# Performance work log

Hardware: AMD Instinct MI355X
Metric: run time of the kernel (lower is better)

The kernel has to match this reference:

```python
import jax, jax.numpy as jnp
import numpy as np

B, H, W, C = 4, 48, 48, 256
NUM_HEADS = 8
DEPTH = C // NUM_HEADS  # 32


def setup_inputs() -> dict:
    key = jax.random.key(0)
    ks = jax.random.split(key, 8)
    scale = 1.0 / np.sqrt(C)
    return {
        "inputs": jax.random.normal(ks[0], (B, H, W, C), dtype=jnp.float32),
        "wq": jax.random.normal(ks[1], (C, C), dtype=jnp.float32) * scale,
        "bq": jax.random.normal(ks[2], (C,), dtype=jnp.float32) * 0.01,
        "wk": jax.random.normal(ks[3], (C, C), dtype=jnp.float32) * scale,
        "bk": jax.random.normal(ks[4], (C,), dtype=jnp.float32) * 0.01,
        "wv": jax.random.normal(ks[5], (C, C), dtype=jnp.float32) * scale,
        "bv": jax.random.normal(ks[6], (C,), dtype=jnp.float32) * 0.01,
        "gamma": jax.random.normal(ks[7], (), dtype=jnp.float32) * 0.1,
    }


def reference(inputs, wq, bq, wk, bk, wv, bv, gamma):
    b, h, w, c = inputs.shape
    n = h * w  # number of tokens

    def proj_split(wm, bm):
        # 1x1 conv == per-pixel dense: [b,h,w,c] @ [c,c] + bias
        y = jnp.einsum('bhwc,cd->bhwd', inputs, wm) + bm
        # split heads -> [b, num_heads, n, depth]
        return y.reshape(b, n, NUM_HEADS, DEPTH).transpose(0, 2, 1, 3)

    q = proj_split(wq, bq) / jnp.sqrt(jnp.asarray(DEPTH, inputs.dtype))
    k = proj_split(wk, bk)
    v = proj_split(wv, bv)

    s = jnp.einsum('bnqd,bnkd->bnqk', q, k)        # [b, heads, n, n]
    a = jax.nn.softmax(s, axis=-1)
    o = jnp.einsum('bnqk,bnkd->bnqd', a, v)        # [b, heads, n, depth]
    o = o.transpose(0, 2, 1, 3).reshape(b, h, w, c)
    return gamma * o + inputs
```

## Files before the change

### kernel.cpp

```cpp
#include <hip/hip_runtime.h>
#include <hip/hip_bf16.h>
#include <cstdint>

#define B_    4
#define NH    8
#define N_TOK 2304
#define D_    32
#define C_    256
#define M_ROWS (B_ * N_TOK)
#define KVB   64
#define NT2   (N_TOK / KVB)
#define M_FIX 10.0f

typedef float  f32x4  __attribute__((ext_vector_type(4)));
typedef short  bf16x8 __attribute__((ext_vector_type(8)));

#define GLOADLDS(g, l) __builtin_amdgcn_global_load_lds( \
    (const __attribute__((address_space(1))) unsigned*)(g), \
    (__attribute__((address_space(3))) unsigned*)(l), 16, 0, 0)

static __device__ __forceinline__ unsigned short f2bf(float f) {
    union { float f; unsigned u; } v; v.f = f;
    unsigned u = v.u;
    u += 0x7FFF + ((u >> 16) & 1);
    return (unsigned short)(u >> 16);
}

static __device__ __forceinline__ unsigned cvt_pk_bf16(float a, float b) {
    unsigned r;
    asm("v_cvt_pk_bf16_f32 %0, %1, %2" : "=v"(r) : "v"(a), "v"(b));
    return r;
}

__global__ void k_prep(const float* __restrict__ x,
                       const float* __restrict__ w0, const float* __restrict__ w1,
                       const float* __restrict__ w2,
                       unsigned short* __restrict__ xb, unsigned short* __restrict__ wt) {
    __shared__ float tile[64][65];
    int bid = blockIdx.x;
    if (bid < 2304) {
        int i = bid * 256 + threadIdx.x;
        float4 v = reinterpret_cast<const float4*>(x)[i];
        ushort4 o;
        o.x = f2bf(v.x); o.y = f2bf(v.y); o.z = f2bf(v.z); o.w = f2bf(v.w);
        reinterpret_cast<ushort4*>(xb)[i] = o;
        return;
    }
    int t   = bid - 2304;
    int mat = t >> 4;  t &= 15;
    const float* w = (mat == 0) ? w0 : (mat == 1) ? w1 : w2;
    int tc  = (t & 3) * 64;
    int td  = (t >> 2) * 64;
    int tid = threadIdx.x;
    int r0  = tid >> 6;
    int x0  = tid & 63;
#pragma unroll
    for (int it = 0; it < 16; ++it) {
        int c = it * 4 + r0;
        tile[c][x0] = w[(tc + c) * C_ + td + x0];
    }
    __syncthreads();
    unsigned short* wto = wt + mat * (C_ * C_);
#pragma unroll
    for (int it = 0; it < 16; ++it) {
        int d = it * 4 + r0;
        wto[(td + d) * C_ + tc + x0] = f2bf(tile[x0][d]);
    }
}

__global__ __launch_bounds__(256) void k_proj(
    const unsigned short* __restrict__ xb,
    const unsigned short* __restrict__ wtb,
    const float* __restrict__ bq, const float* __restrict__ bk, const float* __restrict__ bv,
    unsigned short* __restrict__ qo, unsigned short* __restrict__ kfo, unsigned short* __restrict__ vfo)
{
    __shared__ __align__(16) unsigned short A_lds[3][64][32];
    __shared__ __align__(16) unsigned short B_lds[3][128][32];

    int rows0 = blockIdx.x * 64;
    int cols0 = blockIdx.y * 128;
    int mat   = cols0 >> 8;
    const float* bias = (mat == 0) ? bq : (mat == 1) ? bk : bv;
    float scale = (mat == 0) ? (0.17677669529663687f * 1.4426950408889634f) : 1.0f;

    int tid = threadIdx.x, wave = tid >> 6, lane = tid & 63;
    int lr = lane & 15, lg = lane >> 4;
    int wr = wave >> 1, wc = wave & 1;

    int srow = lane >> 2, sslot = lane & 3;
    int ra   = wave * 16 + srow;
    int keyA = ((ra >> 1) & 1) | (((ra >> 3) & 1) << 1);
    const unsigned short* asrc = xb + (rows0 + ra) * C_ + ((sslot ^ keyA) * 8);
    int rb   = wave * 32 + srow;
    int keyB0 = ((rb >> 1) & 1) | (((rb >> 3) & 1) << 1);
    int keyB1 = (((rb + 16) >> 1) & 1) | ((((rb + 16) >> 3) & 1) << 1);
    const unsigned short* bsrc0 = wtb + (cols0 + rb) * C_ + ((sslot ^ keyB0) * 8);
    const unsigned short* bsrc1 = wtb + (cols0 + rb + 16) * C_ + ((sslot ^ keyB1) * 8);

    char* aldsb = (char*)&A_lds[0][0][0];
    char* bldsb = (char*)&B_lds[0][0][0];
    int adst = wave * 1024;
    int bdst0 = wave * 2048, bdst1 = bdst0 + 1024;

    int xorb = (((lr >> 1) & 1) << 4) | (((lr >> 3) & 1) << 5);
    int fcol = (lg * 16) ^ xorb;
    int arow0 = wr * 32 + lr;
    int brow0 = wc * 64 + lr;

#define PSTAGE(ks, bidx) do {                               \
        int ko_ = (ks) * 32;                                \
        char* ad = aldsb + (bidx) * 4096;                   \
        char* bd = bldsb + (bidx) * 8192;                   \
        GLOADLDS(asrc + ko_, ad + adst);                    \
        GLOADLDS(bsrc0 + ko_, bd + bdst0);                  \
        GLOADLDS(bsrc1 + ko_, bd + bdst1);                  \
    } while (0)

    PSTAGE(0, 0);
    PSTAGE(1, 1);
    asm volatile("s_waitcnt vmcnt(3)" ::: "memory");
    __builtin_amdgcn_s_barrier();

    f32x4 acc[2][4];
#pragma unroll
    for (int i = 0; i < 2; ++i)
#pragma unroll
        for (int j = 0; j < 4; ++j) acc[i][j] = (f32x4){0.f, 0.f, 0.f, 0.f};

    int b0 = 0;
    for (int ks = 0; ks < 8; ++ks) {
        if (ks + 2 < 8) {
            int b2 = b0 + 2; if (b2 >= 3) b2 -= 3;
            PSTAGE(ks + 2, b2);
        }
        const char* ac = aldsb + b0 * 4096;
        const char* bc = bldsb + b0 * 8192;

        bf16x8 a[2], b[4];
#pragma unroll
        for (int fr = 0; fr < 2; ++fr)
            a[fr] = *reinterpret_cast<const bf16x8*>(ac + (arow0 + fr * 16) * 64 + fcol);
#pragma unroll
        for (int fn = 0; fn < 4; ++fn)
            b[fn] = *reinterpret_cast<const bf16x8*>(bc + (brow0 + fn * 16) * 64 + fcol);

        __builtin_amdgcn_s_setprio(1);
#pragma unroll
        for (int fr = 0; fr < 2; ++fr)
#pragma unroll
            for (int fn = 0; fn < 4; ++fn)
                acc[fr][fn] = __builtin_amdgcn_mfma_f32_16x16x32_bf16(a[fr], b[fn], acc[fr][fn], 0, 0, 0);
        __builtin_amdgcn_s_setprio(0);

        if (ks < 7) {
            if (ks + 2 < 8) asm volatile("s_waitcnt vmcnt(3)" ::: "memory");
            else            asm volatile("s_waitcnt vmcnt(0)" ::: "memory");
            __builtin_amdgcn_s_barrier();
        }
        b0 = (b0 + 1 == 3) ? 0 : b0 + 1;
    }
#undef PSTAGE

    int bidx = rows0 / N_TOK;
    int nb   = rows0 - bidx * N_TOK + wr * 32 + lg * 4;

    if (mat == 2) {
#pragma unroll
        for (int fr = 0; fr < 2; ++fr)
#pragma unroll
            for (int fn = 0; fn < 4; ++fn) {
                int cm = (cols0 & 255) + wc * 64 + fn * 16 + lr;
                float bsv = bias[cm];
                int hh = cm >> 5, d = cm & 31;
                int bh = bidx * NH + hh;
                uint2 pr;
                pr.x = cvt_pk_bf16(acc[fr][fn][0] + bsv, acc[fr][fn][1] + bsv);
                pr.y = cvt_pk_bf16(acc[fr][fn][2] + bsv, acc[fr][fn][3] + bsv);
                int n0 = nb + fr * 16;
                int t = n0 >> 6, r = n0 & 63;
                int kseg = r >> 5, lgp = (r >> 3) & 3, i0 = r & 7;
                int c = kseg * 2 + (d >> 4);
                int lV = lgp * 16 + (d & 15);
                *reinterpret_cast<uint2*>(vfo + ((bh * NT2 + t) * 4 + c) * 512 + lV * 8 + i0) = pr;
            }
    } else if (mat == 1) {
#pragma unroll
        for (int fr = 0; fr < 2; ++fr)
#pragma unroll
            for (int fn = 0; fn < 4; ++fn) {
                int cm = (cols0 & 255) + wc * 64 + fn * 16 + lr;
                float bsv = bias[cm];
                int hh = cm >> 5, d = cm & 31;
                int bh = bidx * NH + hh;
#pragma unroll
                for (int j = 0; j < 4; ++j) {
                    int n = nb + fr * 16 + j;
                    int t = n >> 6, r = n & 63;
                    int kt  = ((r >> 5) << 1) | ((r >> 2) & 1);
                    int lr2 = ((r >> 3) & 3) * 4 + (r & 3);
                    int l   = (d >> 3) * 16 + lr2;
                    kfo[((bh * NT2 + t) * 4 + kt) * 512 + l * 8 + (d & 7)] =
                        f2bf(acc[fr][fn][j] + bsv);
                }
            }
    } else {
        unsigned short* dst = qo;
#pragma unroll
        for (int fr = 0; fr < 2; ++fr)
#pragma unroll
            for (int fn = 0; fn < 4; ++fn) {
                int cm = (cols0 & 255) + wc * 64 + fn * 16 + lr;
                float bsv = bias[cm];
                int hh = cm >> 5, d = cm & 31;
#pragma unroll
                for (int j = 0; j < 4; ++j) {
                    float val = (acc[fr][fn][j] + bsv) * scale;
                    dst[((bidx * NH + hh) * N_TOK + nb + fr * 16 + j) * D_ + d] = f2bf(val);
                }
            }
    }
}

__global__ __launch_bounds__(256, 3) void k_attn(
    const unsigned short* __restrict__ qb,
    const unsigned short* __restrict__ kf,
    const unsigned short* __restrict__ vf,
    const float* __restrict__ x,
    const float* __restrict__ gamma_p,
    float* __restrict__ out)
{
    int wid = (blockIdx.x & 7) * 72 + (blockIdx.x >> 3);
    int bh  = wid / 18;
    int qb0 = (wid % 18) * 128;

    int tid = threadIdx.x, wave = tid >> 6, lane = tid & 63;
    int lr = lane & 15, lg = lane >> 4;

    const unsigned short* Q  = qb + bh * N_TOK * D_;
    const unsigned short* Kb = kf + (size_t)bh * (NT2 * 4 * 512) + lane * 8;
    const unsigned short* Vb = vf + (size_t)bh * (NT2 * 4 * 512) + lane * 8;

    int qrowA = qb0 + wave * 32 + lr;
    bf16x8 qA = *reinterpret_cast<const bf16x8*>(Q + qrowA * D_ + lg * 8);
    bf16x8 qB = *reinterpret_cast<const bf16x8*>(Q + (qrowA + 16) * D_ + lg * 8);

#define LDK(dst, t, kt) dst = *reinterpret_cast<const bf16x8*>(Kb + ((t) * 4 + (kt)) * 512)
#define LDV(dst, t, c)  dst = *reinterpret_cast<const bf16x8*>(Vb + ((t) * 4 + (c)) * 512)

    bf16x8 kc0, kc1, kc2, kc3, vc0, vc1, vc2, vc3;
    LDK(kc0, 0, 0); LDK(kc1, 0, 1); LDK(kc2, 0, 2); LDK(kc3, 0, 3);
    LDV(vc0, 0, 0); LDV(vc1, 0, 1); LDV(vc2, 0, 2); LDV(vc3, 0, 3);

    f32x4 accA0 = (f32x4){0.f, 0.f, 0.f, 0.f};
    f32x4 accA1 = (f32x4){0.f, 0.f, 0.f, 0.f};
    f32x4 accB0 = (f32x4){0.f, 0.f, 0.f, 0.f};
    f32x4 accB1 = (f32x4){0.f, 0.f, 0.f, 0.f};
    f32x4 acclA = (f32x4){0.f, 0.f, 0.f, 0.f};
    f32x4 acclB = (f32x4){0.f, 0.f, 0.f, 0.f};

    union { unsigned w[4]; bf16x8 v; } ones;
    ones.w[0] = 0x3F803F80u; ones.w[1] = 0x3F803F80u;
    ones.w[2] = 0x3F803F80u; ones.w[3] = 0x3F803F80u;

    const f32x4 zinit = (f32x4){-M_FIX, -M_FIX, -M_FIX, -M_FIX};

    for (int t = 0; t < NT2; ++t) {
        bf16x8 kn0, kn1, kn2, kn3, vn0, vn1, vn2, vn3;
        if (t + 1 < NT2) {
            LDK(kn0, t + 1, 0); LDK(kn1, t + 1, 1); LDK(kn2, t + 1, 2); LDK(kn3, t + 1, 3);
            LDV(vn0, t + 1, 0); LDV(vn1, t + 1, 1); LDV(vn2, t + 1, 2); LDV(vn3, t + 1, 3);
        }

        f32x4 sA[4], sB[4];
        __builtin_amdgcn_s_setprio(1);
        sA[0] = __builtin_amdgcn_mfma_f32_16x16x32_bf16(kc0, qA, zinit, 0, 0, 0);
        sB[0] = __builtin_amdgcn_mfma_f32_16x16x32_bf16(kc0, qB, zinit, 0, 0, 0);
        sA[1] = __builtin_amdgcn_mfma_f32_16x16x32_bf16(kc1, qA, zinit, 0, 0, 0);
        sB[1] = __builtin_amdgcn_mfma_f32_16x16x32_bf16(kc1, qB, zinit, 0, 0, 0);
        sA[2] = __builtin_amdgcn_mfma_f32_16x16x32_bf16(kc2, qA, zinit, 0, 0, 0);
        sB[2] = __builtin_amdgcn_mfma_f32_16x16x32_bf16(kc2, qB, zinit, 0, 0, 0);
        sA[3] = __builtin_amdgcn_mfma_f32_16x16x32_bf16(kc3, qA, zinit, 0, 0, 0);
        sB[3] = __builtin_amdgcn_mfma_f32_16x16x32_bf16(kc3, qB, zinit, 0, 0, 0);
        __builtin_amdgcn_s_setprio(0);

#pragma unroll
        for (int kseg = 0; kseg < 2; ++kseg) {
            union { unsigned w[4]; bf16x8 v; } paA, paB;
            paA.w[0] = cvt_pk_bf16(__builtin_amdgcn_exp2f(sA[2 * kseg][0]),
                                   __builtin_amdgcn_exp2f(sA[2 * kseg][1]));
            paA.w[1] = cvt_pk_bf16(__builtin_amdgcn_exp2f(sA[2 * kseg][2]),
                                   __builtin_amdgcn_exp2f(sA[2 * kseg][3]));
            paA.w[2] = cvt_pk_bf16(__builtin_amdgcn_exp2f(sA[2 * kseg + 1][0]),
                                   __builtin_amdgcn_exp2f(sA[2 * kseg + 1][1]));
            paA.w[3] = cvt_pk_bf16(__builtin_amdgcn_exp2f(sA[2 * kseg + 1][2]),
                                   __builtin_amdgcn_exp2f(sA[2 * kseg + 1][3]));
            paB.w[0] = cvt_pk_bf16(__builtin_amdgcn_exp2f(sB[2 * kseg][0]),
                                   __builtin_amdgcn_exp2f(sB[2 * kseg][1]));
            paB.w[1] = cvt_pk_bf16(__builtin_amdgcn_exp2f(sB[2 * kseg][2]),
                                   __builtin_amdgcn_exp2f(sB[2 * kseg][3]));
            paB.w[2] = cvt_pk_bf16(__builtin_amdgcn_exp2f(sB[2 * kseg + 1][0]),
                                   __builtin_amdgcn_exp2f(sB[2 * kseg + 1][1]));
            paB.w[3] = cvt_pk_bf16(__builtin_amdgcn_exp2f(sB[2 * kseg + 1][2]),
                                   __builtin_amdgcn_exp2f(sB[2 * kseg + 1][3]));
            bf16x8 vf0 = kseg ? vc2 : vc0;
            bf16x8 vf1 = kseg ? vc3 : vc1;
            accA0 = __builtin_amdgcn_mfma_f32_16x16x32_bf16(paA.v, vf0,    accA0, 0, 0, 0);
            accA1 = __builtin_amdgcn_mfma_f32_16x16x32_bf16(paA.v, vf1,    accA1, 0, 0, 0);
            accB0 = __builtin_amdgcn_mfma_f32_16x16x32_bf16(paB.v, vf0,    accB0, 0, 0, 0);
            accB1 = __builtin_amdgcn_mfma_f32_16x16x32_bf16(paB.v, vf1,    accB1, 0, 0, 0);
            acclA = __builtin_amdgcn_mfma_f32_16x16x32_bf16(paA.v, ones.v, acclA, 0, 0, 0);
            acclB = __builtin_amdgcn_mfma_f32_16x16x32_bf16(paB.v, ones.v, acclB, 0, 0, 0);
        }

        if (t + 1 < NT2) {
            kc0 = kn0; kc1 = kn1; kc2 = kn2; kc3 = kn3;
            vc0 = vn0; vc1 = vn1; vc2 = vn2; vc3 = vn3;
        }
    }
#undef LDK
#undef LDV

    float g = gamma_p[0];
    int b = bh >> 3, head = bh & 7;
#pragma unroll
    for (int j = 0; j < 4; ++j) {
        float linvA = 1.0f / acclA[j];
        float linvB = 1.0f / acclB[j];
        int nA = qb0 + wave * 32 + 4 * lg + j;
        long rA = (long)(b * N_TOK + nA) * C_ + head * 32;
        long rB = rA + 16L * C_;
        out[rA + lr]      = g * (accA0[j] * linvA) + x[rA + lr];
        out[rA + 16 + lr] = g * (accA1[j] * linvA) + x[rA + 16 + lr];
        out[rB + lr]      = g * (accB0[j] * linvB) + x[rB + lr];
        out[rB + 16 + lr] = g * (accB1[j] * linvB) + x[rB + 16 + lr];
    }
}

extern "C" void kernel_launch(void* const* d_in, const int* in_sizes, int n_in,
                              void* d_out, int out_size, void* d_ws, size_t ws_size,
                              hipStream_t stream) {
    const float* x     = (const float*)d_in[0];
    const float* wq    = (const float*)d_in[1];
    const float* bq    = (const float*)d_in[2];
    const float* wk    = (const float*)d_in[3];
    const float* bk    = (const float*)d_in[4];
    const float* wv    = (const float*)d_in[5];
    const float* bv    = (const float*)d_in[6];
    const float* gamma = (const float*)d_in[7];
    float* out = (float*)d_out;

    char* ws = (char*)d_ws;
    unsigned short* xb   = (unsigned short*)(ws);
    unsigned short* wt   = (unsigned short*)(ws + 4718592);
    unsigned short* qbuf = (unsigned short*)(ws + 5111808);
    unsigned short* kfb  = (unsigned short*)(ws + 9830400);
    unsigned short* vfb  = (unsigned short*)(ws + 14548992);

    k_prep<<<dim3(2352), dim3(256), 0, stream>>>(x, wq, wk, wv, xb, wt);
    k_proj<<<dim3(M_ROWS / 64, 6), dim3(256), 0, stream>>>(xb, wt, bq, bk, bv, qbuf, kfb, vfb);
    k_attn<<<dim3(N_TOK / 128 * B_ * NH), dim3(256), 0, stream>>>(qbuf, kfb, vfb, x, gamma, out);
}
```

Before: 59.40 us.

## Split attention KV range across two blocks and combine partials in separate kernel

The attention kernel now splits the key/value sequence into two halves, so it launches twice as many blocks. Each block writes unnormalized partial outputs, the first half in fp32 into the output buffer and the second in bf16 into the reused xb workspace, along with per-row partial softmax sums. A new combine kernel adds the partials, normalizes, and applies gamma and the residual. This is meant to raise occupancy and wave count on the many CUs (576 blocks was a small grid). The cost is an extra launch, extra memory traffic for the partials, and bf16 rounding of one partial. Because exponents use a fixed max, adding the partials directly stays exact.

```diff
diff --git a/kernel.cpp b/kernel.cpp
--- a/kernel.cpp
+++ b/kernel.cpp
@@ -10,6 +10,8 @@
 #define M_ROWS (B_ * N_TOK)
 #define KVB   64
 #define NT2   (N_TOK / KVB)
+#define NSPLIT 2
+#define TPS   (NT2 / NSPLIT)
 #define M_FIX 10.0f
 
 typedef float  f32x4  __attribute__((ext_vector_type(4)));
@@ -225,13 +227,17 @@
     const unsigned short* __restrict__ qb,
     const unsigned short* __restrict__ kf,
     const unsigned short* __restrict__ vf,
-    const float* __restrict__ x,
-    const float* __restrict__ gamma_p,
-    float* __restrict__ out)
+    float* __restrict__ opart,
+    unsigned short* __restrict__ obf,
+    float* __restrict__ lpart)
 {
-    int wid = (blockIdx.x & 7) * 72 + (blockIdx.x >> 3);
-    int bh  = wid / 18;
-    int qb0 = (wid % 18) * 128;
+    int wid = (blockIdx.x & 7) * 144 + (blockIdx.x >> 3);
+    int split = wid / 576;
+    int qid   = wid - split * 576;
+    int bh  = qid / 18;
+    int qb0 = (qid % 18) * 128;
+    int t0   = split * TPS;
+    int tend = t0 + TPS;
 
     int tid = threadIdx.x, wave = tid >> 6, lane = tid & 63;
     int lr = lane & 15, lg = lane >> 4;
@@ -248,8 +254,8 @@
 #define LDV(dst, t, c)  dst = *reinterpret_cast<const bf16x8*>(Vb + ((t) * 4 + (c)) * 512)
 
     bf16x8 kc0, kc1, kc2, kc3, vc0, vc1, vc2, vc3;
-    LDK(kc0, 0, 0); LDK(kc1, 0, 1); LDK(kc2, 0, 2); LDK(kc3, 0, 3);
-    LDV(vc0, 0, 0); LDV(vc1, 0, 1); LDV(vc2, 0, 2); LDV(vc3, 0, 3);
+    LDK(kc0, t0, 0); LDK(kc1, t0, 1); LDK(kc2, t0, 2); LDK(kc3, t0, 3);
+    LDV(vc0, t0, 0); LDV(vc1, t0, 1); LDV(vc2, t0, 2); LDV(vc3, t0, 3);
 
     f32x4 accA0 = (f32x4){0.f, 0.f, 0.f, 0.f};
     f32x4 accA1 = (f32x4){0.f, 0.f, 0.f, 0.f};
@@ -264,9 +270,9 @@
 
     const f32x4 zinit = (f32x4){-M_FIX, -M_FIX, -M_FIX, -M_FIX};
 
-    for (int t = 0; t < NT2; ++t) {
+    for (int t = t0; t < tend; ++t) {
         bf16x8 kn0, kn1, kn2, kn3, vn0, vn1, vn2, vn3;
-        if (t + 1 < NT2) {
+        if (t + 1 < tend) {
             LDK(kn0, t + 1, 0); LDK(kn1, t + 1, 1); LDK(kn2, t + 1, 2); LDK(kn3, t + 1, 3);
             LDV(vn0, t + 1, 0); LDV(vn1, t + 1, 1); LDV(vn2, t + 1, 2); LDV(vn3, t + 1, 3);
         }
@@ -312,7 +318,7 @@
             acclB = __builtin_amdgcn_mfma_f32_16x16x32_bf16(paB.v, ones.v, acclB, 0, 0, 0);
         }
 
-        if (t + 1 < NT2) {
+        if (t + 1 < tend) {
             kc0 = kn0; kc1 = kn1; kc2 = kn2; kc3 = kn3;
             vc0 = vn0; vc1 = vn1; vc2 = vn2; vc3 = vn3;
         }
@@ -320,20 +326,47 @@
 #undef LDK
 #undef LDV
 
-    float g = gamma_p[0];
     int b = bh >> 3, head = bh & 7;
 #pragma unroll
     for (int j = 0; j < 4; ++j) {
-        float linvA = 1.0f / acclA[j];
-        float linvB = 1.0f / acclB[j];
         int nA = qb0 + wave * 32 + 4 * lg + j;
         long rA = (long)(b * N_TOK + nA) * C_ + head * 32;
         long rB = rA + 16L * C_;
-        out[rA + lr]      = g * (accA0[j] * linvA) + x[rA + lr];
-        out[rA + 16 + lr] = g * (accA1[j] * linvA) + x[rA + 16 + lr];
-        out[rB + lr]      = g * (accB0[j] * linvB) + x[rB + lr];
-        out[rB + 16 + lr] = g * (accB1[j] * linvB) + x[rB + 16 + lr];
-    }
+        if (split == 0) {
+            opart[rA + lr]      = accA0[j];
+            opart[rA + 16 + lr] = accA1[j];
+            opart[rB + lr]      = accB0[j];
+            opart[rB + 16 + lr] = accB1[j];
+        } else {
+            obf[rA + lr]      = f2bf(accA0[j]);
+            obf[rA + 16 + lr] = f2bf(accA1[j]);
+            obf[rB + lr]      = f2bf(accB0[j]);
+            obf[rB + 16 + lr] = f2bf(accB1[j]);
+        }
+        if (lr == 0) {
+            float* lp = lpart + split * (32 * N_TOK) + bh * N_TOK;
+            lp[nA]      = acclA[j];
+            lp[nA + 16] = acclB[j];
+        }
+    }
+}
+
+__global__ __launch_bounds__(256) void k_comb(
+    const unsigned short* __restrict__ obf,
+    const float* __restrict__ lpart,
+    const float* __restrict__ x,
+    const float* __restrict__ gamma_p,
+    float* __restrict__ out)
+{
+    int row = blockIdx.x;
+    int c   = threadIdx.x;
+    int b   = row / N_TOK, n = row - b * N_TOK;
+    int head = c >> 5;
+    int bh  = b * NH + head;
+    float l = lpart[bh * N_TOK + n] + lpart[32 * N_TOK + bh * N_TOK + n];
+    long i  = (long)row * C_ + c;
+    float O = out[i] + __uint_as_float(((unsigned)obf[i]) << 16);
+    out[i]  = gamma_p[0] * (O / l) + x[i];
 }
 
 extern "C" void kernel_launch(void* const* d_in, const int* in_sizes, int n_in,
@@ -355,8 +388,11 @@
     unsigned short* qbuf = (unsigned short*)(ws + 5111808);
     unsigned short* kfb  = (unsigned short*)(ws + 9830400);
     unsigned short* vfb  = (unsigned short*)(ws + 14548992);
+    float*          lpt  = (float*)(ws + 19267584);
 
     k_prep<<<dim3(2352), dim3(256), 0, stream>>>(x, wq, wk, wv, xb, wt);
     k_proj<<<dim3(M_ROWS / 64, 6), dim3(256), 0, stream>>>(xb, wt, bq, bk, bv, qbuf, kfb, vfb);
-    k_attn<<<dim3(N_TOK / 128 * B_ * NH), dim3(256), 0, stream>>>(qbuf, kfb, vfb, x, gamma, out);
-}
+    k_attn<<<dim3(N_TOK / 128 * B_ * NH * NSPLIT), dim3(256), 0, stream>>>(
+        qbuf, kfb, vfb, out, xb, lpt);
+    k_comb<<<dim3(M_ROWS), dim3(256), 0, stream>>>(xb, lpt, x, gamma, out);
+}
```

Result: slower. 63.42 us (+6.8%).
